# Optimization experiments

Measured on AMD Instinct MI355X. Metric: run time of the kernel, lower is better.

Reference implementation:

```python
import jax, jax.numpy as jnp
import numpy as np
import math

B, C, DH = 2048, 64, 512
CAP_VOCAB = 11  # max(core_capacities)+1
DIST_VOCAB = 3


def setup_inputs() -> dict:
    key = jax.random.key(0)
    ks = jax.random.split(key, 12)
    inp = {
        "Ht_C": jax.random.normal(ks[0], (B, C, DH), jnp.float32),
        "core_capacities": jax.random.randint(ks[1], (B, C), 0, CAP_VOCAB),
        "distances": jax.random.randint(ks[2], (B, C), 0, DIST_VOCAB),
        "H_X": jax.random.normal(ks[3], (B, DH), jnp.float32),
        "Ht_S": jax.random.normal(ks[4], (B, DH), jnp.float32),
        "Eq_Q": jax.random.normal(ks[5], (B, DH), jnp.float32),
        "double": jax.random.randint(ks[6], (B,), 0, 2).astype(bool),
        # learned parameters (nn.Embedding tables and bias-free Linear weights, [out,in])
        "cap_emb": jax.random.normal(ks[7], (CAP_VOCAB, DH), jnp.float32) * 0.02,
        "dist_emb": jax.random.normal(ks[8], (DIST_VOCAB, DH), jnp.float32) * 0.02,
        "W_q": jax.random.normal(ks[9], (DH, 3 * DH), jnp.float32) * (1.0 / math.sqrt(3 * DH)),
        "W_k": jax.random.normal(ks[10], (DH, DH), jnp.float32) * (1.0 / math.sqrt(DH)),
        "W_v": jax.random.normal(ks[11], (DH, DH), jnp.float32) * (1.0 / math.sqrt(DH)),
    }
    return inp


def reference(Ht_C, core_capacities, distances, H_X, Ht_S, Eq_Q, double,
              cap_emb, dist_emb, W_q, W_k, W_v):
    scale = 1.0 / math.sqrt(Ht_C.shape[-1])  # 1/sqrt(d_H), slice_emb_size == d_H
    # dynamic core embeddings G_{t,q}^{(C)}: [B,C,dH]
    G = Ht_C + cap_emb[core_capacities] + dist_emb[distances]
    # context and projections
    context = jnp.concatenate([H_X, Ht_S, Eq_Q], axis=-1)          # [B,3dH]
    Q = context @ W_q.T                                            # [B,dH]
    K = jnp.einsum('bcd,ed->bce', G, W_k)                          # [B,C,dH]
    V = jnp.einsum('bcd,ed->bce', G, W_v)                          # [B,C,dH]
    # glimpse attention over cores
    attn_logits = jnp.einsum('bcd,bd->bc', K, Q) * scale           # [B,C]
    attn_weights = jax.nn.softmax(attn_logits, axis=-1)            # softmax over cores
    glimpse = jnp.einsum('bc,bcd->bd', attn_weights, V)            # [B,dH]
    # pointer logits + capacity mask
    u = jnp.einsum('bcd,bd->bc', K, glimpse) * scale               # [B,C]
    need = jnp.where(double[:, None], 2, 1)                        # [B,1]
    invalid = core_capacities < need                               # [B,C]
    u = jnp.where(invalid, -jnp.inf, u)
    return jax.nn.softmax(u, axis=-1)                              # [B,C]
```

## Files before the change

### kernel.cpp

```cpp
#include <hip/hip_runtime.h>
#include <math.h>

#define DH 512
#define CC 64
#define NB 2048
#define SCALE 0.044194173824159216f

__device__ __forceinline__ float wsum(float v) {
#pragma unroll
  for (int off = 32; off; off >>= 1) v += __shfl_xor(v, off, 64);
  return v;
}
__device__ __forceinline__ float wmaxf(float v) {
#pragma unroll
  for (int off = 32; off; off >>= 1) v = fmaxf(v, __shfl_xor(v, off, 64));
  return v;
}

__global__ void zero2_kernel(float* __restrict__ p0, float* __restrict__ p1, int n) {
  int i = blockIdx.x * blockDim.x + threadIdx.x;
  int stride = gridDim.x * blockDim.x;
  for (; i < n; i += stride) { p0[i] = 0.f; p1[i] = 0.f; }
}

__global__ void need_kernel(const unsigned char* __restrict__ dbl,
                            int* __restrict__ need) {
  __shared__ int flagNZ, flagFP;
  const int t = threadIdx.x;
  if (t == 0) { flagNZ = 0; flagFP = 0; }
  __syncthreads();
  int nz = 0, fp = 0;
  for (int i = t; i < NB; i += 256) {
    if (i & 3) {
      unsigned char v = dbl[i];
      nz |= (v != 0);
      fp |= (v == 0x3f) | (v == 0x80);
    }
  }
  if (nz) atomicOr(&flagNZ, 1);
  if (fp) atomicOr(&flagFP, 1);
  __syncthreads();
  const int isFP = flagFP, isByte = flagNZ && !flagFP;
  for (int i = t; i < NB; i += 256) {
    int v;
    if (isFP)        v = (((const float*)dbl)[i] != 0.0f);
    else if (isByte) v = (dbl[i] != 0);
    else             v = (((const int*)dbl)[i] != 0);
    need[i] = v ? 2 : 1;
  }
}

#define AS_STR 132

__global__ __launch_bounds__(256) void gemm_nn2(const float* __restrict__ A0,
                                                const float* __restrict__ A1,
                                                const float* __restrict__ A2,
                                                const float* __restrict__ B,
                                                float* __restrict__ C,
                                                int kchunk, int use_atomic) {
  __shared__ float As[16 * AS_STR];
  __shared__ float Bs[16 * 64];
  const int t = threadIdx.x;
  const int m0 = blockIdx.x * 128, n0 = blockIdx.y * 64;
  const int kbeg = blockIdx.z * kchunk, kend = kbeg + kchunk;
  const int tx = t & 15, ty = t >> 4;
  const int ar0 = t >> 2;
  const int ak4 = (t & 3) << 2;
  const int bk = t >> 4, bn4 = (t & 15) << 2;

  float4 ra0, ra1, rb;
  {
    const float* base = (kbeg < 512) ? A0 : ((kbeg < 1024) ? A1 : A2);
    const int kk = kbeg & 511;
    ra0 = *(const float4*)&base[(size_t)(m0 + ar0) * 512 + kk + ak4];
    ra1 = *(const float4*)&base[(size_t)(m0 + ar0 + 64) * 512 + kk + ak4];
    rb  = *(const float4*)&B[(size_t)(kbeg + bk) * 512 + n0 + bn4];
  }
  float acc[8][4] = {};
  for (int k0 = kbeg; k0 < kend; k0 += 16) {
    __syncthreads();
    As[(ak4 + 0) * AS_STR + ar0] = ra0.x;
    As[(ak4 + 1) * AS_STR + ar0] = ra0.y;
    As[(ak4 + 2) * AS_STR + ar0] = ra0.z;
    As[(ak4 + 3) * AS_STR + ar0] = ra0.w;
    As[(ak4 + 0) * AS_STR + ar0 + 64] = ra1.x;
    As[(ak4 + 1) * AS_STR + ar0 + 64] = ra1.y;
    As[(ak4 + 2) * AS_STR + ar0 + 64] = ra1.z;
    As[(ak4 + 3) * AS_STR + ar0 + 64] = ra1.w;
    *(float4*)&Bs[bk * 64 + bn4] = rb;
    __syncthreads();
    if (k0 + 16 < kend) {
      const int kn = k0 + 16;
      const float* base = (kn < 512) ? A0 : ((kn < 1024) ? A1 : A2);
      const int kk = kn & 511;
      ra0 = *(const float4*)&base[(size_t)(m0 + ar0) * 512 + kk + ak4];
      ra1 = *(const float4*)&base[(size_t)(m0 + ar0 + 64) * 512 + kk + ak4];
      rb  = *(const float4*)&B[(size_t)(kn + bk) * 512 + n0 + bn4];
    }
#pragma unroll
    for (int k = 0; k < 16; ++k) {
      float4 a0 = *(float4*)&As[k * AS_STR + (ty << 3)];
      float4 a1 = *(float4*)&As[k * AS_STR + (ty << 3) + 4];
      float4 b  = *(float4*)&Bs[k * 64 + (tx << 2)];
      float av[8] = {a0.x, a0.y, a0.z, a0.w, a1.x, a1.y, a1.z, a1.w};
      float bv[4] = {b.x, b.y, b.z, b.w};
#pragma unroll
      for (int i = 0; i < 8; ++i)
#pragma unroll
        for (int j = 0; j < 4; ++j) acc[i][j] = fmaf(av[i], bv[j], acc[i][j]);
    }
  }
#pragma unroll
  for (int i = 0; i < 8; ++i) {
    float* cp = &C[(size_t)(m0 + (ty << 3) + i) * 512 + n0 + (tx << 2)];
    if (use_atomic) {
      atomicAdd(cp + 0, acc[i][0]);
      atomicAdd(cp + 1, acc[i][1]);
      atomicAdd(cp + 2, acc[i][2]);
      atomicAdd(cp + 3, acc[i][3]);
    } else {
      float4 o = {acc[i][0], acc[i][1], acc[i][2], acc[i][3]};
      *(float4*)cp = o;
    }
  }
}

__global__ __launch_bounds__(256) void gemm_tn2(const float* __restrict__ Wq,
                                                const float* __restrict__ Wv,
                                                const float* __restrict__ Wk,
                                                float* __restrict__ Aout,
                                                float* __restrict__ Mout) {
  __shared__ float As[16 * 128];
  __shared__ float Bs[16 * 64];
  const int t = threadIdx.x;
  const int m0 = blockIdx.x * 128, n0 = blockIdx.y * 64;
  const int tx = t & 15, ty = t >> 4;
  const int ak = t >> 5, am4 = (t & 31) << 2;
  const int bk = t >> 4, bn4 = (t & 15) << 2;
  const bool isQ = (m0 < 1536);
  const float* Acol = isQ ? (Wq + m0) : (Wv + (m0 - 1536));
  const int lda = isQ ? 1536 : 512;
  float* Cout = isQ ? (Aout + (size_t)m0 * 512) : (Mout + (size_t)(m0 - 1536) * 512);

  float4 ra0, ra1, rb;
  ra0 = *(const float4*)&Acol[(size_t)ak * lda + am4];
  ra1 = *(const float4*)&Acol[(size_t)(ak + 8) * lda + am4];
  rb  = *(const float4*)&Wk[(size_t)bk * 512 + n0 + bn4];
  float acc[8][4] = {};
  for (int k0 = 0; k0 < 512; k0 += 16) {
    __syncthreads();
    *(float4*)&As[ak * 128 + am4] = ra0;
    *(float4*)&As[(ak + 8) * 128 + am4] = ra1;
    *(float4*)&Bs[bk * 64 + bn4] = rb;
    __syncthreads();
    if (k0 + 16 < 512) {
      const int kn = k0 + 16;
      ra0 = *(const float4*)&Acol[(size_t)(kn + ak) * lda + am4];
      ra1 = *(const float4*)&Acol[(size_t)(kn + ak + 8) * lda + am4];
      rb  = *(const float4*)&Wk[(size_t)(kn + bk) * 512 + n0 + bn4];
    }
#pragma unroll
    for (int k = 0; k < 16; ++k) {
      float4 a0 = *(float4*)&As[k * 128 + (ty << 3)];
      float4 a1 = *(float4*)&As[k * 128 + (ty << 3) + 4];
      float4 b  = *(float4*)&Bs[k * 64 + (tx << 2)];
      float av[8] = {a0.x, a0.y, a0.z, a0.w, a1.x, a1.y, a1.z, a1.w};
      float bv[4] = {b.x, b.y, b.z, b.w};
#pragma unroll
      for (int i = 0; i < 8; ++i)
#pragma unroll
        for (int j = 0; j < 4; ++j) acc[i][j] = fmaf(av[i], bv[j], acc[i][j]);
    }
  }
#pragma unroll
  for (int i = 0; i < 8; ++i) {
    float4 o = {acc[i][0], acc[i][1], acc[i][2], acc[i][3]};
    *(float4*)&Cout[(size_t)((ty << 3) + i) * 512 + n0 + (tx << 2)] = o;
  }
}

__global__ __launch_bounds__(256) void pass1_kernel(const float* __restrict__ HtC,
                                                    const int* __restrict__ caps,
                                                    const int* __restrict__ dists,
                                                    const float* __restrict__ Qk,
                                                    const float* __restrict__ cap_emb,
                                                    const float* __restrict__ dist_emb,
                                                    float* __restrict__ Gw) {
  const int b = blockIdx.x;
  const int t = threadIdx.x;
  const int wv = t >> 6, ln = t & 63;
  __shared__ float qk[DH];
  __shared__ float capQ[11], distQ[3];
  __shared__ float capw[11], distw[3];
  __shared__ float logits[CC];
  __shared__ float wts[CC];
  if (t < 11) capw[t] = 0.f;
  if (t < 3) distw[t] = 0.f;
  qk[t] = Qk[(size_t)b * DH + t];
  qk[t + 256] = Qk[(size_t)b * DH + 256 + t];
  __syncthreads();
#pragma unroll
  for (int r = 0; r < 3; ++r) {
    int v = wv + (r << 2);
    if (v < 11) {
      float s = 0.f;
#pragma unroll
      for (int j = 0; j < 8; ++j) s = fmaf(cap_emb[v * DH + ln + (j << 6)], qk[ln + (j << 6)], s);
      s = wsum(s);
      if (ln == 0) capQ[v] = s;
    }
  }
  if (wv < 3) {
    float s = 0.f;
#pragma unroll
    for (int j = 0; j < 8; ++j) s = fmaf(dist_emb[wv * DH + ln + (j << 6)], qk[ln + (j << 6)], s);
    s = wsum(s);
    if (ln == 0) distQ[wv] = s;
  }
  __syncthreads();
  const float4* qk4 = (const float4*)qk;
  float4 q1 = qk4[ln];
  float4 q2 = qk4[64 + ln];
  const float* hb = HtC + (size_t)b * CC * DH;
#pragma unroll 4
  for (int i = 0; i < 16; ++i) {
    int c = (wv << 4) + i;
    const float4* h4 = (const float4*)(hb + (size_t)c * DH);
    float4 h1 = h4[ln];
    float4 h2 = h4[64 + ln];
    float s = h1.x * q1.x + h1.y * q1.y + h1.z * q1.z + h1.w * q1.w +
              h2.x * q2.x + h2.y * q2.y + h2.z * q2.z + h2.w * q2.w;
    s = wsum(s);
    if (ln == 0)
      logits[c] = SCALE * (s + capQ[caps[b * CC + c]] + distQ[dists[b * CC + c]]);
  }
  __syncthreads();
  if (t < CC) {
    float x = logits[t];
    float m = wmaxf(x);
    float e = __expf(x - m);
    float ssum = wsum(e);
    float w = e / ssum;
    wts[t] = w;
    atomicAdd(&capw[caps[b * CC + t]], w);
    atomicAdd(&distw[dists[b * CC + t]], w);
  }
  __syncthreads();
#pragma unroll
  for (int dd = 0; dd < 2; ++dd) {
    int d = t + (dd << 8);
    float g = 0.f;
#pragma unroll 8
    for (int c = 0; c < CC; ++c) g = fmaf(wts[c], hb[(size_t)c * DH + d], g);
#pragma unroll
    for (int v = 0; v < 11; ++v) g = fmaf(capw[v], cap_emb[v * DH + d], g);
#pragma unroll
    for (int v = 0; v < 3; ++v) g = fmaf(distw[v], dist_emb[v * DH + d], g);
    Gw[(size_t)b * DH + d] = g;
  }
}

__global__ __launch_bounds__(256) void pass2_kernel(const float* __restrict__ HtC,
                                                    const int* __restrict__ caps,
                                                    const int* __restrict__ dists,
                                                    const float* __restrict__ gkv,
                                                    const float* __restrict__ cap_emb,
                                                    const float* __restrict__ dist_emb,
                                                    const int* __restrict__ need,
                                                    float* __restrict__ out) {
  const int b = blockIdx.x;
  const int t = threadIdx.x;
  const int wv = t >> 6, ln = t & 63;
  __shared__ float gk[DH];
  __shared__ float capG[11], distG[3];
  __shared__ float ulog[CC];
  gk[t] = gkv[(size_t)b * DH + t];
  gk[t + 256] = gkv[(size_t)b * DH + 256 + t];
  __syncthreads();
#pragma unroll
  for (int r = 0; r < 3; ++r) {
    int v = wv + (r << 2);
    if (v < 11) {
      float s = 0.f;
#pragma unroll
      for (int j = 0; j < 8; ++j) s = fmaf(cap_emb[v * DH + ln + (j << 6)], gk[ln + (j << 6)], s);
      s = wsum(s);
      if (ln == 0) capG[v] = s;
    }
  }
  if (wv < 3) {
    float s = 0.f;
#pragma unroll
    for (int j = 0; j < 8; ++j) s = fmaf(dist_emb[wv * DH + ln + (j << 6)], gk[ln + (j << 6)], s);
    s = wsum(s);
    if (ln == 0) distG[wv] = s;
  }
  __syncthreads();
  const float4* gk4 = (const float4*)gk;
  float4 q1 = gk4[ln];
  float4 q2 = gk4[64 + ln];
  const float* hb = HtC + (size_t)b * CC * DH;
#pragma unroll 4
  for (int i = 0; i < 16; ++i) {
    int c = (wv << 4) + i;
    const float4* h4 = (const float4*)(hb + (size_t)c * DH);
    float4 h1 = h4[ln];
    float4 h2 = h4[64 + ln];
    float s = h1.x * q1.x + h1.y * q1.y + h1.z * q1.z + h1.w * q1.w +
              h2.x * q2.x + h2.y * q2.y + h2.z * q2.z + h2.w * q2.w;
    s = wsum(s);
    if (ln == 0)
      ulog[c] = SCALE * (s + capG[caps[b * CC + c]] + distG[dists[b * CC + c]]);
  }
  __syncthreads();
  if (t < CC) {
    int nb = need[b];
    float x = ulog[t];
    if (caps[b * CC + t] < nb) x = -INFINITY;
    float m = wmaxf(x);
    float e = __expf(x - m);
    float ssum = wsum(e);
    out[(size_t)b * CC + t] = e / ssum;
  }
}

extern "C" void kernel_launch(void* const* d_in, const int* in_sizes, int n_in,
                              void* d_out, int out_size, void* d_ws, size_t ws_size,
                              hipStream_t stream) {
  const float* HtC      = (const float*)d_in[0];
  const int* caps       = (const int*)d_in[1];
  const int* dists      = (const int*)d_in[2];
  const float* H_X      = (const float*)d_in[3];
  const float* Ht_S     = (const float*)d_in[4];
  const float* Eq_Q     = (const float*)d_in[5];
  const unsigned char* dbl = (const unsigned char*)d_in[6];
  const float* cap_emb  = (const float*)d_in[7];
  const float* dist_emb = (const float*)d_in[8];
  const float* W_q      = (const float*)d_in[9];
  const float* W_k      = (const float*)d_in[10];
  const float* W_v      = (const float*)d_in[11];
  float* out = (float*)d_out;

  float* ws    = (float*)d_ws;
  float* wsA   = ws;
  float* wsM   = wsA + 1536 * 512;
  float* wsQk  = wsM + 512 * 512;
  float* wsGw  = wsQk + 2048 * 512;
  float* wsGk  = wsGw + 2048 * 512;
  int* wsNeed  = (int*)(wsGk + 2048 * 512);

  zero2_kernel<<<512, 256, 0, stream>>>(wsQk, wsGk, 2048 * 512);
  need_kernel<<<1, 256, 0, stream>>>(dbl, wsNeed);
  gemm_tn2<<<dim3(16, 8), 256, 0, stream>>>(W_q, W_v, W_k, wsA, wsM);
  gemm_nn2<<<dim3(16, 8, 4), 256, 0, stream>>>(H_X, Ht_S, Eq_Q, wsA, wsQk, 384, 1);
  pass1_kernel<<<NB, 256, 0, stream>>>(HtC, caps, dists, wsQk, cap_emb, dist_emb, wsGw);
  gemm_nn2<<<dim3(16, 8, 2), 256, 0, stream>>>(wsGw, wsGw, wsGw, wsM, wsGk, 256, 1);
  pass2_kernel<<<NB, 256, 0, stream>>>(HtC, caps, dists, wsGk, cap_emb, dist_emb, wsNeed, out);
}
```

Baseline: 638.1 us.

## Fuse glimpse accumulation into single HtC pass and replace split-K atomics with partials

pass1 now accumulates exp-weighted HtC rows in registers while computing logits, so HtC is read once instead of twice in that kernel. Normalization is deferred and the softmax max subtraction is dropped. Split-K GEMMs write per-split partial buffers that the consumer kernels sum, which removes the zeroing kernel and the atomics. The need computation is folded into the weight-precompute GEMM launch, cutting two kernel launches. Skipping the max subtraction risks overflow if logits grow large.

```diff
diff --git a/kernel.cpp b/kernel.cpp
--- a/kernel.cpp
+++ b/kernel.cpp
@@ -11,58 +11,107 @@
   for (int off = 32; off; off >>= 1) v += __shfl_xor(v, off, 64);
   return v;
 }
-__device__ __forceinline__ float wmaxf(float v) {
-#pragma unroll
-  for (int off = 32; off; off >>= 1) v = fmaxf(v, __shfl_xor(v, off, 64));
-  return v;
-}
-
-__global__ void zero2_kernel(float* __restrict__ p0, float* __restrict__ p1, int n) {
-  int i = blockIdx.x * blockDim.x + threadIdx.x;
-  int stride = gridDim.x * blockDim.x;
-  for (; i < n; i += stride) { p0[i] = 0.f; p1[i] = 0.f; }
-}
-
-__global__ void need_kernel(const unsigned char* __restrict__ dbl,
-                            int* __restrict__ need) {
-  __shared__ int flagNZ, flagFP;
+
+__global__ __launch_bounds__(128) void pre_kernel(const float* __restrict__ Wq,
+                                                  const float* __restrict__ Wv,
+                                                  const float* __restrict__ Wk,
+                                                  float* __restrict__ Aout,
+                                                  float* __restrict__ Mout,
+                                                  const unsigned char* __restrict__ dbl,
+                                                  int* __restrict__ need) {
+  const int bx = blockIdx.x;
   const int t = threadIdx.x;
-  if (t == 0) { flagNZ = 0; flagFP = 0; }
-  __syncthreads();
-  int nz = 0, fp = 0;
-  for (int i = t; i < NB; i += 256) {
-    if (i & 3) {
-      unsigned char v = dbl[i];
-      nz |= (v != 0);
-      fp |= (v == 0x3f) | (v == 0x80);
-    }
-  }
-  if (nz) atomicOr(&flagNZ, 1);
-  if (fp) atomicOr(&flagFP, 1);
-  __syncthreads();
-  const int isFP = flagFP, isByte = flagNZ && !flagFP;
-  for (int i = t; i < NB; i += 256) {
-    int v;
-    if (isFP)        v = (((const float*)dbl)[i] != 0.0f);
-    else if (isByte) v = (dbl[i] != 0);
-    else             v = (((const int*)dbl)[i] != 0);
-    need[i] = v ? 2 : 1;
+  if (bx == 256) {
+    __shared__ int flagNZ, flagFP;
+    if (t == 0) { flagNZ = 0; flagFP = 0; }
+    __syncthreads();
+    int nz = 0, fp = 0;
+    for (int i = t; i < NB; i += 128) {
+      if (i & 3) {
+        unsigned char v = dbl[i];
+        nz |= (v != 0);
+        fp |= (v == 0x3f) | (v == 0x80);
+      }
+    }
+    if (nz) atomicOr(&flagNZ, 1);
+    if (fp) atomicOr(&flagFP, 1);
+    __syncthreads();
+    const int isFP = flagFP, isByte = flagNZ && !flagFP;
+    for (int i = t; i < NB; i += 128) {
+      int v;
+      if (isFP)        v = (((const float*)dbl)[i] != 0.0f);
+      else if (isByte) v = (dbl[i] != 0);
+      else             v = (((const int*)dbl)[i] != 0);
+      need[i] = v ? 2 : 1;
+    }
+    return;
+  }
+  __shared__ float As[16][64];
+  __shared__ float Bs[16][64];
+  const int mt = bx >> 3, nt = bx & 7;
+  const int m0 = mt * 64, n0 = nt * 64;
+  const bool isQ = (m0 < 1536);
+  const float* Acol = isQ ? (Wq + m0) : (Wv + (m0 - 1536));
+  const int lda = isQ ? 1536 : 512;
+  float* Cout = isQ ? (Aout + (size_t)m0 * 512) : (Mout + (size_t)(m0 - 1536) * 512);
+  const int lr = t >> 3;
+  const int lc = (t & 7) << 3;
+  const int tx = t & 15, ty = t >> 4;
+
+  float4 ra0, ra1, rb0, rb1;
+  ra0 = *(const float4*)&Acol[(size_t)lr * lda + lc];
+  ra1 = *(const float4*)&Acol[(size_t)lr * lda + lc + 4];
+  rb0 = *(const float4*)&Wk[(size_t)lr * 512 + n0 + lc];
+  rb1 = *(const float4*)&Wk[(size_t)lr * 512 + n0 + lc + 4];
+  float acc[8][4] = {};
+  for (int k0 = 0; k0 < 512; k0 += 16) {
+    __syncthreads();
+    *(float4*)&As[lr][lc] = ra0;
+    *(float4*)&As[lr][lc + 4] = ra1;
+    *(float4*)&Bs[lr][lc] = rb0;
+    *(float4*)&Bs[lr][lc + 4] = rb1;
+    __syncthreads();
+    if (k0 + 16 < 512) {
+      const int kn = k0 + 16 + lr;
+      ra0 = *(const float4*)&Acol[(size_t)kn * lda + lc];
+      ra1 = *(const float4*)&Acol[(size_t)kn * lda + lc + 4];
+      rb0 = *(const float4*)&Wk[(size_t)kn * 512 + n0 + lc];
+      rb1 = *(const float4*)&Wk[(size_t)kn * 512 + n0 + lc + 4];
+    }
+#pragma unroll
+    for (int k = 0; k < 16; ++k) {
+      float4 a0 = *(float4*)&As[k][ty << 3];
+      float4 a1 = *(float4*)&As[k][(ty << 3) + 4];
+      float4 b  = *(float4*)&Bs[k][tx << 2];
+      float av[8] = {a0.x, a0.y, a0.z, a0.w, a1.x, a1.y, a1.z, a1.w};
+      float bv[4] = {b.x, b.y, b.z, b.w};
+#pragma unroll
+      for (int i = 0; i < 8; ++i)
+#pragma unroll
+        for (int j = 0; j < 4; ++j) acc[i][j] = fmaf(av[i], bv[j], acc[i][j]);
+    }
+  }
+#pragma unroll
+  for (int i = 0; i < 8; ++i) {
+    float4 o = {acc[i][0], acc[i][1], acc[i][2], acc[i][3]};
+    *(float4*)&Cout[(size_t)((ty << 3) + i) * 512 + n0 + (tx << 2)] = o;
   }
 }
 
 #define AS_STR 132
 
-__global__ __launch_bounds__(256) void gemm_nn2(const float* __restrict__ A0,
-                                                const float* __restrict__ A1,
-                                                const float* __restrict__ A2,
-                                                const float* __restrict__ B,
-                                                float* __restrict__ C,
-                                                int kchunk, int use_atomic) {
+__global__ __launch_bounds__(256) void gemm_nn2p(const float* __restrict__ A0,
+                                                 const float* __restrict__ A1,
+                                                 const float* __restrict__ A2,
+                                                 const float* __restrict__ B,
+                                                 float* __restrict__ Cp,
+                                                 int kchunk) {
   __shared__ float As[16 * AS_STR];
   __shared__ float Bs[16 * 64];
   const int t = threadIdx.x;
   const int m0 = blockIdx.x * 128, n0 = blockIdx.y * 64;
   const int kbeg = blockIdx.z * kchunk, kend = kbeg + kchunk;
+  float* C = Cp + (size_t)blockIdx.z * (NB * DH);
   const int tx = t & 15, ty = t >> 4;
   const int ar0 = t >> 2;
   const int ak4 = (t & 3) << 2;
@@ -112,77 +161,15 @@
   }
 #pragma unroll
   for (int i = 0; i < 8; ++i) {
-    float* cp = &C[(size_t)(m0 + (ty << 3) + i) * 512 + n0 + (tx << 2)];
-    if (use_atomic) {
-      atomicAdd(cp + 0, acc[i][0]);
-      atomicAdd(cp + 1, acc[i][1]);
-      atomicAdd(cp + 2, acc[i][2]);
-      atomicAdd(cp + 3, acc[i][3]);
-    } else {
-      float4 o = {acc[i][0], acc[i][1], acc[i][2], acc[i][3]};
-      *(float4*)cp = o;
-    }
-  }
-}
-
-__global__ __launch_bounds__(256) void gemm_tn2(const float* __restrict__ Wq,
-                                                const float* __restrict__ Wv,
-                                                const float* __restrict__ Wk,
-                                                float* __restrict__ Aout,
-                                                float* __restrict__ Mout) {
-  __shared__ float As[16 * 128];
-  __shared__ float Bs[16 * 64];
-  const int t = threadIdx.x;
-  const int m0 = blockIdx.x * 128, n0 = blockIdx.y * 64;
-  const int tx = t & 15, ty = t >> 4;
-  const int ak = t >> 5, am4 = (t & 31) << 2;
-  const int bk = t >> 4, bn4 = (t & 15) << 2;
-  const bool isQ = (m0 < 1536);
-  const float* Acol = isQ ? (Wq + m0) : (Wv + (m0 - 1536));
-  const int lda = isQ ? 1536 : 512;
-  float* Cout = isQ ? (Aout + (size_t)m0 * 512) : (Mout + (size_t)(m0 - 1536) * 512);
-
-  float4 ra0, ra1, rb;
-  ra0 = *(const float4*)&Acol[(size_t)ak * lda + am4];
-  ra1 = *(const float4*)&Acol[(size_t)(ak + 8) * lda + am4];
-  rb  = *(const float4*)&Wk[(size_t)bk * 512 + n0 + bn4];
-  float acc[8][4] = {};
-  for (int k0 = 0; k0 < 512; k0 += 16) {
-    __syncthreads();
-    *(float4*)&As[ak * 128 + am4] = ra0;
-    *(float4*)&As[(ak + 8) * 128 + am4] = ra1;
-    *(float4*)&Bs[bk * 64 + bn4] = rb;
-    __syncthreads();
-    if (k0 + 16 < 512) {
-      const int kn = k0 + 16;
-      ra0 = *(const float4*)&Acol[(size_t)(kn + ak) * lda + am4];
-      ra1 = *(const float4*)&Acol[(size_t)(kn + ak + 8) * lda + am4];
-      rb  = *(const float4*)&Wk[(size_t)(kn + bk) * 512 + n0 + bn4];
-    }
-#pragma unroll
-    for (int k = 0; k < 16; ++k) {
-      float4 a0 = *(float4*)&As[k * 128 + (ty << 3)];
-      float4 a1 = *(float4*)&As[k * 128 + (ty << 3) + 4];
-      float4 b  = *(float4*)&Bs[k * 64 + (tx << 2)];
-      float av[8] = {a0.x, a0.y, a0.z, a0.w, a1.x, a1.y, a1.z, a1.w};
-      float bv[4] = {b.x, b.y, b.z, b.w};
-#pragma unroll
-      for (int i = 0; i < 8; ++i)
-#pragma unroll
-        for (int j = 0; j < 4; ++j) acc[i][j] = fmaf(av[i], bv[j], acc[i][j]);
-    }
-  }
-#pragma unroll
-  for (int i = 0; i < 8; ++i) {
     float4 o = {acc[i][0], acc[i][1], acc[i][2], acc[i][3]};
-    *(float4*)&Cout[(size_t)((ty << 3) + i) * 512 + n0 + (tx << 2)] = o;
+    *(float4*)&C[(size_t)(m0 + (ty << 3) + i) * 512 + n0 + (tx << 2)] = o;
   }
 }
 
 __global__ __launch_bounds__(256) void pass1_kernel(const float* __restrict__ HtC,
                                                     const int* __restrict__ caps,
                                                     const int* __restrict__ dists,
-                                                    const float* __restrict__ Qk,
+                                                    const float* __restrict__ Qkp,
                                                     const float* __restrict__ cap_emb,
                                                     const float* __restrict__ dist_emb,
                                                     float* __restrict__ Gw) {
@@ -191,13 +178,22 @@
   const int wv = t >> 6, ln = t & 63;
   __shared__ float qk[DH];
   __shared__ float capQ[11], distQ[3];
-  __shared__ float capw[11], distw[3];
-  __shared__ float logits[CC];
-  __shared__ float wts[CC];
-  if (t < 11) capw[t] = 0.f;
-  if (t < 3) distw[t] = 0.f;
-  qk[t] = Qk[(size_t)b * DH + t];
-  qk[t + 256] = Qk[(size_t)b * DH + 256 + t];
+  __shared__ float capE[11], distE[3];
+  __shared__ float ec[CC];
+  __shared__ float accs[4][DH];
+  __shared__ float lsum_s;
+  if (t < 11) capE[t] = 0.f;
+  if (t < 3) distE[t] = 0.f;
+  {
+    float q0 = 0.f, q1 = 0.f;
+#pragma unroll
+    for (int z = 0; z < 4; ++z) {
+      q0 += Qkp[(size_t)z * NB * DH + (size_t)b * DH + t];
+      q1 += Qkp[(size_t)z * NB * DH + (size_t)b * DH + 256 + t];
+    }
+    qk[t] = q0;
+    qk[t + 256] = q1;
+  }
   __syncthreads();
 #pragma unroll
   for (int r = 0; r < 3; ++r) {
@@ -222,6 +218,7 @@
   float4 q1 = qk4[ln];
   float4 q2 = qk4[64 + ln];
   const float* hb = HtC + (size_t)b * CC * DH;
+  float a0 = 0.f, a1 = 0.f, a2 = 0.f, a3 = 0.f, a4 = 0.f, a5 = 0.f, a6 = 0.f, a7 = 0.f;
 #pragma unroll 4
   for (int i = 0; i < 16; ++i) {
     int c = (wv << 4) + i;
@@ -231,39 +228,47 @@
     float s = h1.x * q1.x + h1.y * q1.y + h1.z * q1.z + h1.w * q1.w +
               h2.x * q2.x + h2.y * q2.y + h2.z * q2.z + h2.w * q2.w;
     s = wsum(s);
-    if (ln == 0)
-      logits[c] = SCALE * (s + capQ[caps[b * CC + c]] + distQ[dists[b * CC + c]]);
+    float logit = SCALE * (s + capQ[caps[b * CC + c]] + distQ[dists[b * CC + c]]);
+    float e = __expf(logit);
+    if (ln == 0) ec[c] = e;
+    a0 = fmaf(e, h1.x, a0); a1 = fmaf(e, h1.y, a1);
+    a2 = fmaf(e, h1.z, a2); a3 = fmaf(e, h1.w, a3);
+    a4 = fmaf(e, h2.x, a4); a5 = fmaf(e, h2.y, a5);
+    a6 = fmaf(e, h2.z, a6); a7 = fmaf(e, h2.w, a7);
+  }
+  {
+    int d0 = ln << 2;
+    accs[wv][d0 + 0] = a0; accs[wv][d0 + 1] = a1;
+    accs[wv][d0 + 2] = a2; accs[wv][d0 + 3] = a3;
+    accs[wv][256 + d0 + 0] = a4; accs[wv][256 + d0 + 1] = a5;
+    accs[wv][256 + d0 + 2] = a6; accs[wv][256 + d0 + 3] = a7;
   }
   __syncthreads();
   if (t < CC) {
-    float x = logits[t];
-    float m = wmaxf(x);
-    float e = __expf(x - m);
-    float ssum = wsum(e);
-    float w = e / ssum;
-    wts[t] = w;
-    atomicAdd(&capw[caps[b * CC + t]], w);
-    atomicAdd(&distw[dists[b * CC + t]], w);
-  }
-  __syncthreads();
+    float e = ec[t];
+    float l = wsum(e);
+    if (t == 0) lsum_s = l;
+    atomicAdd(&capE[caps[b * CC + t]], e);
+    atomicAdd(&distE[dists[b * CC + t]], e);
+  }
+  __syncthreads();
+  const float rinv = 1.0f / lsum_s;
 #pragma unroll
   for (int dd = 0; dd < 2; ++dd) {
     int d = t + (dd << 8);
-    float g = 0.f;
-#pragma unroll 8
-    for (int c = 0; c < CC; ++c) g = fmaf(wts[c], hb[(size_t)c * DH + d], g);
-#pragma unroll
-    for (int v = 0; v < 11; ++v) g = fmaf(capw[v], cap_emb[v * DH + d], g);
-#pragma unroll
-    for (int v = 0; v < 3; ++v) g = fmaf(distw[v], dist_emb[v * DH + d], g);
-    Gw[(size_t)b * DH + d] = g;
+    float g = accs[0][d] + accs[1][d] + accs[2][d] + accs[3][d];
+#pragma unroll
+    for (int v = 0; v < 11; ++v) g = fmaf(capE[v], cap_emb[v * DH + d], g);
+#pragma unroll
+    for (int v = 0; v < 3; ++v) g = fmaf(distE[v], dist_emb[v * DH + d], g);
+    Gw[(size_t)b * DH + d] = g * rinv;
   }
 }
 
 __global__ __launch_bounds__(256) void pass2_kernel(const float* __restrict__ HtC,
                                                     const int* __restrict__ caps,
                                                     const int* __restrict__ dists,
-                                                    const float* __restrict__ gkv,
+                                                    const float* __restrict__ Gkp,
                                                     const float* __restrict__ cap_emb,
                                                     const float* __restrict__ dist_emb,
                                                     const int* __restrict__ need,
@@ -274,8 +279,12 @@
   __shared__ float gk[DH];
   __shared__ float capG[11], distG[3];
   __shared__ float ulog[CC];
-  gk[t] = gkv[(size_t)b * DH + t];
-  gk[t + 256] = gkv[(size_t)b * DH + 256 + t];
+  {
+    float g0 = Gkp[(size_t)b * DH + t] + Gkp[(size_t)NB * DH + (size_t)b * DH + t];
+    float g1 = Gkp[(size_t)b * DH + 256 + t] + Gkp[(size_t)NB * DH + (size_t)b * DH + 256 + t];
+    gk[t] = g0;
+    gk[t + 256] = g1;
+  }
   __syncthreads();
 #pragma unroll
   for (int r = 0; r < 3; ++r) {
@@ -317,7 +326,9 @@
     int nb = need[b];
     float x = ulog[t];
     if (caps[b * CC + t] < nb) x = -INFINITY;
-    float m = wmaxf(x);
+    float m = x;
+#pragma unroll
+    for (int off = 32; off; off >>= 1) m = fmaxf(m, __shfl_xor(m, off, 64));
     float e = __expf(x - m);
     float ssum = wsum(e);
     out[(size_t)b * CC + t] = e / ssum;
@@ -341,19 +352,17 @@
   const float* W_v      = (const float*)d_in[11];
   float* out = (float*)d_out;
 
-  float* ws    = (float*)d_ws;
-  float* wsA   = ws;
-  float* wsM   = wsA + 1536 * 512;
-  float* wsQk  = wsM + 512 * 512;
-  float* wsGw  = wsQk + 2048 * 512;
-  float* wsGk  = wsGw + 2048 * 512;
-  int* wsNeed  = (int*)(wsGk + 2048 * 512);
-
-  zero2_kernel<<<512, 256, 0, stream>>>(wsQk, wsGk, 2048 * 512);
-  need_kernel<<<1, 256, 0, stream>>>(dbl, wsNeed);
-  gemm_tn2<<<dim3(16, 8), 256, 0, stream>>>(W_q, W_v, W_k, wsA, wsM);
-  gemm_nn2<<<dim3(16, 8, 4), 256, 0, stream>>>(H_X, Ht_S, Eq_Q, wsA, wsQk, 384, 1);
-  pass1_kernel<<<NB, 256, 0, stream>>>(HtC, caps, dists, wsQk, cap_emb, dist_emb, wsGw);
-  gemm_nn2<<<dim3(16, 8, 2), 256, 0, stream>>>(wsGw, wsGw, wsGw, wsM, wsGk, 256, 1);
-  pass2_kernel<<<NB, 256, 0, stream>>>(HtC, caps, dists, wsGk, cap_emb, dist_emb, wsNeed, out);
-}
+  float* ws     = (float*)d_ws;
+  float* wsA    = ws;
+  float* wsM    = wsA + 1536 * 512;
+  float* wsQkp  = wsM + 512 * 512;
+  float* wsGw   = wsQkp + 4 * 2048 * 512;
+  float* wsGkp  = wsGw + 2048 * 512;
+  int* wsNeed   = (int*)(wsGkp + 2 * 2048 * 512);
+
+  pre_kernel<<<257, 128, 0, stream>>>(W_q, W_v, W_k, wsA, wsM, dbl, wsNeed);
+  gemm_nn2p<<<dim3(16, 8, 4), 256, 0, stream>>>(H_X, Ht_S, Eq_Q, wsA, wsQkp, 384);
+  pass1_kernel<<<NB, 256, 0, stream>>>(HtC, caps, dists, wsQkp, cap_emb, dist_emb, wsGw);
+  gemm_nn2p<<<dim3(16, 8, 2), 256, 0, stream>>>(wsGw, wsGw, wsGw, wsM, wsGkp, 256);
+  pass2_kernel<<<NB, 256, 0, stream>>>(HtC, caps, dists, wsGkp, cap_emb, dist_emb, wsNeed, out);
+}
```

Result: faster. 530.2 us (-16.9%).
